# Performance work log

Measured on AMD Instinct MI355X. Metric: run time of the kernel, lower is better.

The kernel has to match this reference:

```python
import jax, jax.numpy as jnp
import numpy as np

N_NODES = 50000
N_EDGES = 800000
IN_DIM = 64
OUT_DIM = 64


def setup_inputs() -> dict:
    key = jax.random.key(0)
    ks = jax.random.split(key, 10)
    v = jax.random.normal(ks[0], (N_NODES, IN_DIM), jnp.float32)
    src = jax.random.randint(ks[1], (N_EDGES,), 0, N_NODES, dtype=jnp.int32)
    dst = jax.random.randint(ks[2], (N_EDGES,), 0, N_NODES, dtype=jnp.int32)

    def xavier(k, shape, fan_in, fan_out):
        std = np.sqrt(2.0 / (fan_in + fan_out)).astype(np.float32)
        return jax.random.normal(k, shape, jnp.float32) * std

    # Linear weights stored transposed relative to torch: x @ W, W: [in, out]
    Wa = xavier(ks[3], (IN_DIM, OUT_DIM), IN_DIM, OUT_DIM)
    att_l = xavier(ks[4], (OUT_DIM,), OUT_DIM, 1)
    att_r = xavier(ks[5], (OUT_DIM,), OUT_DIM, 1)
    gate_l = xavier(ks[6], (IN_DIM,), IN_DIM, 1)
    gate_m = xavier(ks[7], (OUT_DIM,), OUT_DIM, 1)
    gate_r = xavier(ks[8], (IN_DIM,), IN_DIM, 1)
    Wgm = xavier(ks[9], (IN_DIM, OUT_DIM), IN_DIM, OUT_DIM)
    return {"v": v, "src": src, "dst": dst, "Wa": Wa, "att_l": att_l,
            "att_r": att_r, "gate_l": gate_l, "gate_m": gate_m,
            "gate_r": gate_r, "Wgm": Wgm}


def reference(v, src, dst, Wa, att_l, att_r, gate_l, gate_m, gate_r, Wgm):
    N = v.shape[0]
    # proj_z = z = Wa(v)  (attention projection, also the residual branch)
    z = v @ Wa                                   # [N, OUT]
    el = z @ att_l                               # [N]  att_out_fc_l(z)
    er = z @ att_r                               # [N]  att_out_fc_r(z)
    # edge attention: leaky_relu(el[src] + er[dst]), slope 0.01 (torch default)
    e = jax.nn.leaky_relu(el[src] + er[dst], negative_slope=0.01)  # [E]
    # segment softmax over incoming edges of each dst node
    emax = jax.ops.segment_max(e, dst, num_segments=N)
    emax = jnp.where(jnp.isfinite(emax), emax, 0.0)  # guard empty segments
    ex = jnp.exp(e - emax[dst])
    esum = jax.ops.segment_sum(ex, dst, num_segments=N)
    alpha = ex / esum[dst]                       # [E]
    # h = sum_j alpha_ij * proj_z_j    (dropout on alpha omitted: deterministic ref)
    h = jax.ops.segment_sum(alpha[:, None] * z[src], dst, num_segments=N)  # [N, OUT]
    # gate: max over Wgm(v_src), mean over v_src, per dst node
    gproj = v @ Wgm                              # [N, OUT] (node-level == per-edge Wgm(v_src))
    deg = jax.ops.segment_sum(jnp.ones_like(e), dst, num_segments=N)       # [N]
    gmax = jax.ops.segment_max(gproj[src], dst, num_segments=N)
    gmax = jnp.where((deg > 0)[:, None], gmax, 0.0)
    vmean = jax.ops.segment_sum(v[src], dst, num_segments=N) / jnp.maximum(deg, 1.0)[:, None]
    gval = jax.nn.sigmoid(v @ gate_l + gmax @ gate_m + vmean @ gate_r)     # [N]
    h = gval[:, None] * h
    return z + h
```

## Files before the change

### kernel.cpp

```cpp
#include <hip/hip_runtime.h>
#include <hip/hip_bf16.h>
#include <math.h>

#define N_NODES 50000
#define N_EDGES 800000
#define DIM 64
#define CAP 96
#define CSTRIDE 16

__device__ __forceinline__ float wave_reduce_sum(float x) {
#pragma unroll
  for (int off = 32; off > 0; off >>= 1) x += __shfl_xor(x, off, 64);
  return x;
}

__device__ __forceinline__ unsigned int f2bf_bits(float x) {
  unsigned int u = __float_as_uint(x);
  return (u + 0x7fffu + ((u >> 16) & 1u)) >> 16;
}

__global__ __launch_bounds__(256) void k_fused(
    const float* __restrict__ v, const float* __restrict__ Wa,
    const float* __restrict__ att_l, const float* __restrict__ att_r,
    const float* __restrict__ gate_l, const float* __restrict__ gate_r,
    const float* __restrict__ Wgm,
    const int* __restrict__ src, const int* __restrict__ dst,
    unsigned int* __restrict__ zg, float2* __restrict__ elgr,
    float* __restrict__ erv, float* __restrict__ glv,
    int* __restrict__ cursor, int* __restrict__ rec)
{
  const int t = threadIdx.x;

  {
    const int i = blockIdx.x * 256 + t;
    const int s = src[i], d = dst[i];
    const int p = atomicAdd(&cursor[d * CSTRIDE], 1);
    if (p < CAP) rec[d * CAP + p] = s;
  }

  __shared__ float4 vL[16 * 16];
  const int nb = blockIdx.x * 16;
  vL[t] = ((const float4*)v)[nb * 16 + t];
  __syncthreads();

  const int wave = t >> 6, lane = t & 63;
  const float glw = gate_l[lane], grw = gate_r[lane];

#pragma unroll
  for (int it = 0; it < 4; ++it) {
    const int nl = wave * 4 + it;
    const float vj = ((const float*)vL)[nl * 64 + lane];
    const float gl_ = wave_reduce_sum(vj * glw);
    const float gr_ = wave_reduce_sum(vj * grw);
    if (lane == 0) { glv[nb + nl] = gl_; elgr[nb + nl].y = gr_; }
  }

  float wa[DIM], wg[DIM];
#pragma unroll
  for (int k = 0; k < DIM; ++k) {
    wa[k] = Wa[k * DIM + lane];
    wg[k] = Wgm[k * DIM + lane];
  }
  const float al = att_l[lane], ar = att_r[lane];

#pragma unroll
  for (int it = 0; it < 4; ++it) {
    const int nl = wave * 4 + it;
    const int n = nb + nl;
    float z0 = 0.f, z1 = 0.f, g0 = 0.f, g1 = 0.f;
#pragma unroll
    for (int j = 0; j < 16; ++j) {
      const float4 vv = vL[nl * 16 + j];
      z0 = fmaf(vv.x, wa[4 * j + 0], z0);
      g0 = fmaf(vv.x, wg[4 * j + 0], g0);
      z1 = fmaf(vv.y, wa[4 * j + 1], z1);
      g1 = fmaf(vv.y, wg[4 * j + 1], g1);
      z0 = fmaf(vv.z, wa[4 * j + 2], z0);
      g0 = fmaf(vv.z, wg[4 * j + 2], g0);
      z1 = fmaf(vv.w, wa[4 * j + 3], z1);
      g1 = fmaf(vv.w, wg[4 * j + 3], g1);
    }
    const float zj = z0 + z1, gj = g0 + g1;
    const float el_ = wave_reduce_sum(zj * al);
    const float er_ = wave_reduce_sum(zj * ar);
    zg[n * DIM + lane] = (f2bf_bits(zj) << 16) | f2bf_bits(gj);
    if (lane == 0) { elgr[n].x = el_; erv[n] = er_; }
  }
}

__global__ __launch_bounds__(256) void k_aggregate(
    const int* __restrict__ cursor, const int* __restrict__ rec,
    const float2* __restrict__ elgr, const float* __restrict__ erv,
    const float* __restrict__ glv, const unsigned int* __restrict__ zg,
    const float* __restrict__ gate_m, float* __restrict__ out)
{
  __shared__ float2 sw[4][64];
  const int wave = threadIdx.x >> 6, lane = threadIdx.x & 63;
  const int n = blockIdx.x * 4 + wave;
  int deg = cursor[n * CSTRIDE];
  deg = (deg < CAP) ? deg : CAP;
  const int base = n * CAP;
  const float er_n = erv[n];
  const unsigned int zres_u = zg[n * DIM + lane];
  const float gmw = gate_m[lane];
  const float glv_n = glv[n];

  float sum_ex = 0.f, sum_gr = 0.f, hv = 0.f, gm = -INFINITY;

  for (int b = 0; b < deg; b += 64) {
    const int m = (deg - b < 64) ? (deg - b) : 64;

    int s_l = 0; float ex_l = 0.f;
    if (lane < m) {
      s_l = rec[base + b + lane];
      const float2 eg = elgr[s_l];
      float ev = eg.x + er_n;
      ev = (ev > 0.f) ? ev : 0.01f * ev;
      ex_l = __expf(ev);
      sum_ex += ex_l;
      sum_gr += eg.y;
    }
    sw[wave][lane] = make_float2(__int_as_float(s_l), ex_l);

    int j = 0;
    for (; j + 16 <= m; j += 16) {
      float2 q[16];
      unsigned int a[16];
#pragma unroll
      for (int k = 0; k < 16; ++k) q[k] = sw[wave][j + k];
#pragma unroll
      for (int k = 0; k < 16; ++k) a[k] = zg[__float_as_int(q[k].x) * DIM + lane];
#pragma unroll
      for (int k = 0; k < 16; ++k) {
        hv = fmaf(q[k].y, __uint_as_float(a[k] & 0xffff0000u), hv);
        gm = fmaxf(gm, __uint_as_float(a[k] << 16));
      }
    }
    for (; j + 4 <= m; j += 4) {
      float2 q[4];
      unsigned int a[4];
#pragma unroll
      for (int k = 0; k < 4; ++k) q[k] = sw[wave][j + k];
#pragma unroll
      for (int k = 0; k < 4; ++k) a[k] = zg[__float_as_int(q[k].x) * DIM + lane];
#pragma unroll
      for (int k = 0; k < 4; ++k) {
        hv = fmaf(q[k].y, __uint_as_float(a[k] & 0xffff0000u), hv);
        gm = fmaxf(gm, __uint_as_float(a[k] << 16));
      }
    }
    for (; j < m; ++j) {
      const float2 q = sw[wave][j];
      const unsigned int a = zg[__float_as_int(q.x) * DIM + lane];
      hv = fmaf(q.y, __uint_as_float(a & 0xffff0000u), hv);
      gm = fmaxf(gm, __uint_as_float(a << 16));
    }
  }

  sum_ex = wave_reduce_sum(sum_ex);
  sum_gr = wave_reduce_sum(sum_gr);
  const float inv = (deg > 0) ? 1.f / sum_ex : 0.f;
  hv *= inv;

  const float gmv = (deg > 0) ? gm : 0.f;
  const float dot = wave_reduce_sum(gmv * gmw);
  const float x = glv_n + dot + sum_gr / fmaxf((float)deg, 1.f);
  const float gval = 1.f / (1.f + expf(-x));
  const float zres = __uint_as_float(zres_u & 0xffff0000u);
  out[n * DIM + lane] = zres + gval * hv;
}

extern "C" void kernel_launch(void* const* d_in, const int* in_sizes, int n_in,
                              void* d_out, int out_size, void* d_ws, size_t ws_size,
                              hipStream_t stream) {
  const float* v      = (const float*)d_in[0];
  const int*   src    = (const int*)d_in[1];
  const int*   dst    = (const int*)d_in[2];
  const float* Wa     = (const float*)d_in[3];
  const float* att_l  = (const float*)d_in[4];
  const float* att_r  = (const float*)d_in[5];
  const float* gate_l = (const float*)d_in[6];
  const float* gate_m = (const float*)d_in[7];
  const float* gate_r = (const float*)d_in[8];
  const float* Wgm    = (const float*)d_in[9];
  float* out = (float*)d_out;

  unsigned int* zg = (unsigned int*)d_ws;
  float2* elgr = (float2*)(zg + N_NODES * DIM);
  float* erv   = (float*)(elgr + N_NODES);
  float* glv   = erv + N_NODES;
  int* cursor  = (int*)(glv + N_NODES);
  int* rec     = cursor + N_NODES * CSTRIDE;

  hipMemsetAsync(cursor, 0, N_NODES * CSTRIDE * sizeof(int), stream);

  k_fused<<<3125, 256, 0, stream>>>(v, Wa, att_l, att_r, gate_l, gate_r, Wgm,
                                    src, dst, zg, elgr, erv, glv, cursor, rec);
  k_aggregate<<<12500, 256, 0, stream>>>(cursor, rec, elgr, erv, glv, zg, gate_m, out);
}
```

Before: 170.2 us.

## Replace per-node atomic bucketing with two-pass binned partition into compact CSR

Edge bucketing no longer does one global atomic per edge into fixed per-node slots. It now runs in two passes. First, edges are binned into 256 ranges of 196 destination nodes, with shared-memory counting and one global atomic per bin per block. Then each bin is turned into a compact CSR in shared memory using a prefix scan. The aim is to cut global atomic contention, drop the large padded cursor memset, and give the aggregate kernel contiguous neighbor lists. It adds two more kernel launches and an intermediate pairs buffer. A bin overflowing SEGCAP would silently drop edges.

Measured after the change: 171.5 us. No clear change (+0.7%).

```diff
diff --git a/kernel.cpp b/kernel.cpp
--- a/kernel.cpp
+++ b/kernel.cpp
@@ -5,8 +5,12 @@
 #define N_NODES 50000
 #define N_EDGES 800000
 #define DIM 64
-#define CAP 96
-#define CSTRIDE 16
+#define RW 196
+#define NR 256
+#define SEGCAP 4096
+#define NB1 196
+#define EPB1 4096
+#define CPAD 16
 
 __device__ __forceinline__ float wave_reduce_sum(float x) {
 #pragma unroll
@@ -19,25 +23,45 @@
   return (u + 0x7fffu + ((u >> 16) & 1u)) >> 16;
 }
 
-__global__ __launch_bounds__(256) void k_fused(
+__global__ __launch_bounds__(256) void k_part1(
+    const int* __restrict__ src, const int* __restrict__ dst,
+    int* __restrict__ segcur, int2* __restrict__ pairs)
+{
+  __shared__ int2 pr[EPB1];
+  __shared__ int cnt[NR], gb[NR], lcur[NR];
+  const int t = threadIdx.x;
+  cnt[t] = 0; lcur[t] = 0;
+  __syncthreads();
+#pragma unroll
+  for (int k = 0; k < EPB1 / 256; ++k) {
+    const int i = blockIdx.x * EPB1 + k * 256 + t;
+    int d = -1, s = 0;
+    if (i < N_EDGES) { d = dst[i]; s = src[i]; atomicAdd(&cnt[(unsigned)d / RW], 1); }
+    pr[k * 256 + t] = make_int2(d, s);
+  }
+  __syncthreads();
+  gb[t] = atomicAdd(&segcur[t * CPAD], cnt[t]);
+  __syncthreads();
+#pragma unroll
+  for (int k = 0; k < EPB1 / 256; ++k) {
+    const int2 p = pr[k * 256 + t];
+    if (p.x >= 0) {
+      const int bin = (unsigned)p.x / RW;
+      const int l = gb[bin] + atomicAdd(&lcur[bin], 1);
+      if (l < SEGCAP) pairs[bin * SEGCAP + l] = p;
+    }
+  }
+}
+
+__global__ __launch_bounds__(256) void k_proj(
     const float* __restrict__ v, const float* __restrict__ Wa,
     const float* __restrict__ att_l, const float* __restrict__ att_r,
     const float* __restrict__ gate_l, const float* __restrict__ gate_r,
     const float* __restrict__ Wgm,
-    const int* __restrict__ src, const int* __restrict__ dst,
     unsigned int* __restrict__ zg, float2* __restrict__ elgr,
-    float* __restrict__ erv, float* __restrict__ glv,
-    int* __restrict__ cursor, int* __restrict__ rec)
+    float* __restrict__ erv, float* __restrict__ glv)
 {
   const int t = threadIdx.x;
-
-  {
-    const int i = blockIdx.x * 256 + t;
-    const int s = src[i], d = dst[i];
-    const int p = atomicAdd(&cursor[d * CSTRIDE], 1);
-    if (p < CAP) rec[d * CAP + p] = s;
-  }
-
   __shared__ float4 vL[16 * 16];
   const int nb = blockIdx.x * 16;
   vL[t] = ((const float4*)v)[nb * 16 + t];
@@ -88,8 +112,55 @@
   }
 }
 
+__global__ __launch_bounds__(256) void k_part2(
+    const int* __restrict__ segcur, const int2* __restrict__ pairs,
+    int* __restrict__ csr, int* __restrict__ offs, int* __restrict__ degv)
+{
+  __shared__ int2 pr[SEGCAP];
+  __shared__ int cnt[256], sc[256], lcur[256];
+  const int t = threadIdx.x;
+  const int rb = blockIdx.x;
+  const int lo = rb * RW;
+  int tot = segcur[rb * CPAD];
+  tot = (tot < SEGCAP) ? tot : SEGCAP;
+  cnt[t] = 0; lcur[t] = 0;
+  __syncthreads();
+#pragma unroll
+  for (int k = 0; k < SEGCAP / 256; ++k) {
+    const int j = k * 256 + t;
+    int2 p = make_int2(-1, 0);
+    if (j < tot) { p = pairs[rb * SEGCAP + j]; atomicAdd(&cnt[p.x - lo], 1); }
+    pr[j] = p;
+  }
+  __syncthreads();
+  const int x = cnt[t];
+  sc[t] = x;
+  __syncthreads();
+  for (int off = 1; off < 256; off <<= 1) {
+    const int tmp = (t >= off) ? sc[t - off] : 0;
+    __syncthreads();
+    sc[t] += tmp;
+    __syncthreads();
+  }
+  const int bs = sc[t] - x;
+  const int n = lo + t;
+  if (t < RW && n < N_NODES) { offs[n] = rb * SEGCAP + bs; degv[n] = x; }
+  sc[t] = bs;
+  __syncthreads();
+#pragma unroll
+  for (int k = 0; k < SEGCAP / 256; ++k) {
+    const int2 p = pr[k * 256 + t];
+    if (p.x >= 0) {
+      const int b = p.x - lo;
+      const int l = atomicAdd(&lcur[b], 1);
+      csr[rb * SEGCAP + sc[b] + l] = p.y;
+    }
+  }
+}
+
 __global__ __launch_bounds__(256) void k_aggregate(
-    const int* __restrict__ cursor, const int* __restrict__ rec,
+    const int* __restrict__ offs, const int* __restrict__ degv,
+    const int* __restrict__ csr,
     const float2* __restrict__ elgr, const float* __restrict__ erv,
     const float* __restrict__ glv, const unsigned int* __restrict__ zg,
     const float* __restrict__ gate_m, float* __restrict__ out)
@@ -97,9 +168,8 @@
   __shared__ float2 sw[4][64];
   const int wave = threadIdx.x >> 6, lane = threadIdx.x & 63;
   const int n = blockIdx.x * 4 + wave;
-  int deg = cursor[n * CSTRIDE];
-  deg = (deg < CAP) ? deg : CAP;
-  const int base = n * CAP;
+  const int deg = degv[n];
+  const int base = offs[n];
   const float er_n = erv[n];
   const unsigned int zres_u = zg[n * DIM + lane];
   const float gmw = gate_m[lane];
@@ -112,7 +182,7 @@
 
     int s_l = 0; float ex_l = 0.f;
     if (lane < m) {
-      s_l = rec[base + b + lane];
+      s_l = csr[base + b + lane];
       const float2 eg = elgr[s_l];
       float ev = eg.x + er_n;
       ev = (ev > 0.f) ? ev : 0.01f * ev;
@@ -185,16 +255,21 @@
   const float* Wgm    = (const float*)d_in[9];
   float* out = (float*)d_out;
 
-  unsigned int* zg = (unsigned int*)d_ws;
+  int2* pairs  = (int2*)d_ws;
+  unsigned int* zg = (unsigned int*)(pairs + NR * SEGCAP);
   float2* elgr = (float2*)(zg + N_NODES * DIM);
   float* erv   = (float*)(elgr + N_NODES);
   float* glv   = erv + N_NODES;
-  int* cursor  = (int*)(glv + N_NODES);
-  int* rec     = cursor + N_NODES * CSTRIDE;
-
-  hipMemsetAsync(cursor, 0, N_NODES * CSTRIDE * sizeof(int), stream);
-
-  k_fused<<<3125, 256, 0, stream>>>(v, Wa, att_l, att_r, gate_l, gate_r, Wgm,
-                                    src, dst, zg, elgr, erv, glv, cursor, rec);
-  k_aggregate<<<12500, 256, 0, stream>>>(cursor, rec, elgr, erv, glv, zg, gate_m, out);
-}
+  int* csr     = (int*)(glv + N_NODES);
+  int* offs    = csr + NR * SEGCAP;
+  int* degv    = offs + N_NODES;
+  int* segcur  = degv + N_NODES;
+
+  hipMemsetAsync(segcur, 0, NR * CPAD * sizeof(int), stream);
+
+  k_part1<<<NB1, 256, 0, stream>>>(src, dst, segcur, pairs);
+  k_proj<<<3125, 256, 0, stream>>>(v, Wa, att_l, att_r, gate_l, gate_r, Wgm,
+                                   zg, elgr, erv, glv);
+  k_part2<<<NR, 256, 0, stream>>>(segcur, pairs, csr, offs, degv);
+  k_aggregate<<<12500, 256, 0, stream>>>(offs, degv, csr, elgr, erv, glv, zg, gate_m, out);
+}
```
